# Optimization experiments

Hardware: AMD Instinct MI355X
Metric: run time of the kernel (lower is better)

## Reference

```python
import jax, jax.numpy as jnp
import numpy as np

B, H, W = 16, 352, 352
EPS = 1e-7

# Directable[TL_table[i]] for i = 0..7: (dx, dy), dx=+1 shifts right, dy=+1 shifts down
# TL_table = [lower_right, down, lower_left, right, left, upper_right, up, upper_left]
SHIFTS = [(1, 1), (0, 1), (-1, 1), (1, 0), (-1, 0), (1, -1), (0, -1), (-1, -1)]


def _shift(x, dx, dy):
    # x: [B,H,W]; zero-padded translation, equivalent to the bmm against the
    # near-identity translation matrices in the original code.
    if dx == 1:
        x = jnp.pad(x, ((0, 0), (0, 0), (1, 0)))[:, :, :-1]
    elif dx == -1:
        x = jnp.pad(x, ((0, 0), (0, 0), (0, 1)))[:, :, 1:]
    if dy == 1:
        x = jnp.pad(x, ((0, 0), (1, 0), (0, 0)))[:, :-1, :]
    elif dy == -1:
        x = jnp.pad(x, ((0, 0), (0, 1), (0, 0)))[:, 1:, :]
    return x


def _bce_sum(p, t):
    p = jnp.clip(p, EPS, 1.0 - EPS)
    return -jnp.sum(t * jnp.log(p) + (1.0 - t) * jnp.log1p(-p))


def setup_inputs() -> dict:
    key = jax.random.key(0)
    k1, k2, k3 = jax.random.split(key, 3)
    c_map = jax.random.normal(k1, (B, 8, H, W), dtype=jnp.float32)
    target = jax.random.uniform(k2, (B, 1, H, W), dtype=jnp.float32)
    con_target = jax.random.randint(k3, (B, 8, H, W), 0, 2, dtype=jnp.int32)
    return {"c_map": c_map, "target": target, "con_target": con_target}


def reference(c_map, target, con_target):
    p = jax.nn.sigmoid(c_map)                      # [B,8,H,W]
    con = con_target.astype(p.dtype)
    sum_conn = jnp.sum(con, axis=1)                # [B,H,W]
    edge = ((sum_conn < 8) & (sum_conn > 0)).astype(p.dtype)

    # Bilateral voting: shifted[:, i] = shift(p[:, 7-i], direction_i)
    shifted = jnp.stack(
        [_shift(p[:, 7 - i], *SHIFTS[i]) for i in range(8)], axis=1
    )                                              # [B,8,H,W]
    vote = p * shifted                             # [B,8,H,W]

    glo_map = jnp.max(vote, axis=1)                # [B,H,W]
    pred_mask_min = jnp.min(vote, axis=1)          # [B,H,W]
    decouple = glo_map * (1.0 - edge) + (1.0 - pred_mask_min) * edge

    de_loss = _bce_sum(decouple[:, None], target)
    conmap_l = _bce_sum(p, con)
    bimap_l = _bce_sum(vote, con)
    return 0.8 * conmap_l + de_loss + 0.2 * bimap_l
```

## Files before the change

### kernel.cpp

```cpp
#include <hip/hip_runtime.h>


#define EPSF 1e-7f

constexpr int B = 16, H = 352, W = 352;
constexpr int HW = H * W;
constexpr int N = B * HW;
constexpr int W4 = W / 4;
constexpr int HW4 = HW / 4;
constexpr int NQ = N / 4;
constexpr int NBLK = NQ / 256;

typedef float f4 __attribute__((ext_vector_type(4)));
typedef int   i4 __attribute__((ext_vector_type(4)));

__device__ __forceinline__ float rcpf(float x) { return __builtin_amdgcn_rcpf(x); }

__device__ __forceinline__ f4 sigmoid4(f4 x) {
    f4 r;
    r.x = rcpf(1.0f + __expf(-x.x));
    r.y = rcpf(1.0f + __expf(-x.y));
    r.z = rcpf(1.0f + __expf(-x.z));
    r.w = rcpf(1.0f + __expf(-x.w));
    return r;
}
__device__ __forceinline__ f4 max4(f4 a, f4 b) {
    f4 r; r.x=fmaxf(a.x,b.x); r.y=fmaxf(a.y,b.y); r.z=fmaxf(a.z,b.z); r.w=fmaxf(a.w,b.w); return r;
}
__device__ __forceinline__ f4 min4(f4 a, f4 b) {
    f4 r; r.x=fminf(a.x,b.x); r.y=fminf(a.y,b.y); r.z=fminf(a.z,b.z); r.w=fminf(a.w,b.w); return r;
}
__device__ __forceinline__ f4 sel4(i4 q, f4 a, f4 b) {
    f4 r; r.x=q.x?a.x:b.x; r.y=q.y?a.y:b.y; r.z=q.z?a.z:b.z; r.w=q.w?a.w:b.w; return r;
}
__device__ __forceinline__ f4 loadu4(const float* p) {
    f4 v; __builtin_memcpy(&v, p, sizeof(f4)); return v;
}

__device__ __forceinline__ float finish_pixel(float glo, float pmin, int sc,
                                              float t, float cp, float ba, float bb) {
    const float edge = (sc < 8 && sc > 0) ? 1.0f : 0.0f;
    float dec = glo * (1.0f - edge) + (1.0f - pmin) * edge;
    dec = fminf(fmaxf(dec, EPSF), 1.0f - EPSF);
    const float de = -(t * __logf(dec) + (1.0f - t) * __logf(1.0f - dec));
    return de - 0.8f * __logf(cp) - 0.2f * (__logf(ba) + __logf(bb));
}

__global__ __launch_bounds__(256, 4) void bicon_loss_kernel(
    const float* __restrict__ c_map,
    const float* __restrict__ target,
    const int*   __restrict__ con,
    float* __restrict__ ws)
{
    const int tid = blockIdx.x * blockDim.x + threadIdx.x;
    const int b  = tid / HW4;
    const int rq = tid - b * HW4;
    const int y  = rq / W4;
    const int xq = rq - y * W4;
    const int x0 = xq * 4;

    const float* __restrict__ cm = c_map + (size_t)b * 8 * HW + y * W + x0;
    const int*   __restrict__ cn = con   + (size_t)b * 8 * HW + y * W + x0;

    const f4 c0 = *(const f4*)(cm + 0 * HW);
    const f4 c1 = *(const f4*)(cm + 1 * HW);
    const f4 c2 = *(const f4*)(cm + 2 * HW);
    const f4 c3 = *(const f4*)(cm + 3 * HW);
    const f4 c4 = *(const f4*)(cm + 4 * HW);
    const f4 c5 = *(const f4*)(cm + 5 * HW);
    const f4 c6 = *(const f4*)(cm + 6 * HW);
    const f4 c7 = *(const f4*)(cm + 7 * HW);
    const f4 n0 = loadu4(cm + 7 * HW - 1 * W - 1);
    const f4 n1 = *(const f4*)(cm + 6 * HW - 1 * W);
    const f4 n2 = loadu4(cm + 5 * HW - 1 * W + 1);
    const f4 n3 = loadu4(cm + 4 * HW - 1);
    const f4 n4 = loadu4(cm + 3 * HW + 1);
    const f4 n5 = loadu4(cm + 2 * HW + 1 * W - 1);
    const f4 n6 = *(const f4*)(cm + 1 * HW + 1 * W);
    const f4 n7 = loadu4(cm + 0 * HW + 1 * W + 1);
    const i4 q0 = *(const i4*)(cn + 0 * HW);
    const i4 q1 = *(const i4*)(cn + 1 * HW);
    const i4 q2 = *(const i4*)(cn + 2 * HW);
    const i4 q3 = *(const i4*)(cn + 3 * HW);
    const i4 q4 = *(const i4*)(cn + 4 * HW);
    const i4 q5 = *(const i4*)(cn + 5 * HW);
    const i4 q6 = *(const i4*)(cn + 6 * HW);
    const i4 q7 = *(const i4*)(cn + 7 * HW);
    const f4 t4 = *(const f4*)(target + (size_t)b * HW + y * W + x0);

    const f4 p0 = sigmoid4(c0);
    const f4 p1 = sigmoid4(c1);
    const f4 p2 = sigmoid4(c2);
    const f4 p3 = sigmoid4(c3);
    const f4 p4 = sigmoid4(c4);
    const f4 p5 = sigmoid4(c5);
    const f4 p6 = sigmoid4(c6);
    const f4 p7 = sigmoid4(c7);

    const float lm = (xq == 0)      ? 0.0f : 1.0f;
    const float rm = (xq == W4 - 1) ? 0.0f : 1.0f;
    const float tm = (y == 0)       ? 0.0f : 1.0f;
    const float bm = (y == H - 1)   ? 0.0f : 1.0f;

    f4 conprod = {1.f,1.f,1.f,1.f};
    f4 biA     = {1.f,1.f,1.f,1.f};
    f4 biB     = {1.f,1.f,1.f,1.f};
    f4 glo     = {-1e30f,-1e30f,-1e30f,-1e30f};
    f4 pmin    = { 1e30f, 1e30f, 1e30f, 1e30f};

#define DIR(P, Q, NR, DX, RMASK, BI) {                                        \
        f4 s = sigmoid4(NR);                                                  \
        s *= (RMASK);                                                         \
        if ((DX) == 1)  s.x *= lm;                                            \
        if ((DX) == -1) s.w *= rm;                                            \
        const f4 v = (P) * s;                                                 \
        glo  = max4(glo,  v);                                                 \
        pmin = min4(pmin, v);                                                 \
        conprod *= sel4((Q), (P), 1.0f - (P));                                \
        BI *= sel4((Q), max4(v, (f4){EPSF,EPSF,EPSF,EPSF}), 1.0f - v);        \
    }
    DIR(p0, q0, n0,  1, tm, biA)
    DIR(p1, q1, n1,  0, tm, biA)
    DIR(p2, q2, n2, -1, tm, biA)
    DIR(p3, q3, n3,  1, 1.0f, biA)
    DIR(p4, q4, n4, -1, 1.0f, biB)
    DIR(p5, q5, n5,  1, bm, biB)
    DIR(p6, q6, n6,  0, bm, biB)
    DIR(p7, q7, n7, -1, bm, biB)
#undef DIR

    const i4 sc = q0 + q1 + q2 + q3 + q4 + q5 + q6 + q7;

    float part = finish_pixel(glo.x, pmin.x, sc.x, t4.x, conprod.x, biA.x, biB.x)
               + finish_pixel(glo.y, pmin.y, sc.y, t4.y, conprod.y, biA.y, biB.y)
               + finish_pixel(glo.z, pmin.z, sc.z, t4.z, conprod.z, biA.z, biB.z)
               + finish_pixel(glo.w, pmin.w, sc.w, t4.w, conprod.w, biA.w, biB.w);

    #pragma unroll
    for (int off = 32; off > 0; off >>= 1)
        part += __shfl_down(part, off, 64);

    __shared__ float wsum[4];
    const int lane = threadIdx.x & 63;
    const int wid  = threadIdx.x >> 6;
    if (lane == 0) wsum[wid] = part;
    __syncthreads();
    if (threadIdx.x == 0) {
        ws[blockIdx.x] = wsum[0] + wsum[1] + wsum[2] + wsum[3];
    }
}

__global__ __launch_bounds__(256) void reduce_partials_kernel(
    const float* __restrict__ ws, float* __restrict__ out)
{
    float s = 0.0f;
    for (int i = threadIdx.x; i < NBLK; i += 256) s += ws[i];
    #pragma unroll
    for (int off = 32; off > 0; off >>= 1)
        s += __shfl_down(s, off, 64);
    __shared__ float wsum[4];
    const int lane = threadIdx.x & 63;
    const int wid  = threadIdx.x >> 6;
    if (lane == 0) wsum[wid] = s;
    __syncthreads();
    if (threadIdx.x == 0) out[0] = wsum[0] + wsum[1] + wsum[2] + wsum[3];
}

extern "C" void kernel_launch(void* const* d_in, const int* in_sizes, int n_in,
                              void* d_out, int out_size, void* d_ws, size_t ws_size,
                              hipStream_t stream) {
    const float* c_map  = (const float*)d_in[0];
    const float* target = (const float*)d_in[1];
    const int*   con    = (const int*)d_in[2];
    float* out = (float*)d_out;
    float* ws  = (float*)d_ws;

    bicon_loss_kernel<<<NBLK, 256, 0, stream>>>(c_map, target, con, ws);
    reduce_partials_kernel<<<1, 256, 0, stream>>>(ws, out);
}
```

Before: 149.4 us.

## Process four-row strips per thread with rolling sigmoid window and lane shuffles

Each thread now walks four consecutive rows instead of one pixel quad. Sigmoid values for the previous, current and next rows are carried in registers and reused across rows, so each input element gets its sigmoid once instead of twice. Horizontal neighbours come from cross-lane shuffles, with scalar fix-up loads only at wavefront edges, replacing the unaligned global loads. The trade-off is a grid four times smaller (484 blocks), which means less latency hiding and more register pressure per thread.

Measured after the change: 167.4 us. +12.1%, slower.

```diff
diff --git a/kernel.cpp b/kernel.cpp
--- a/kernel.cpp
+++ b/kernel.cpp
@@ -3,18 +3,21 @@
 
 #define EPSF 1e-7f
 
-constexpr int B = 16, H = 352, W = 352;
+constexpr int B_ = 16, H = 352, W = 352;
 constexpr int HW = H * W;
-constexpr int N = B * HW;
 constexpr int W4 = W / 4;
-constexpr int HW4 = HW / 4;
-constexpr int NQ = N / 4;
-constexpr int NBLK = NQ / 256;
+constexpr int RPT = 4;
+constexpr int STRIPS = H / RPT;
+constexpr int SPB = STRIPS * W4;
+constexpr int NT = B_ * SPB;
+constexpr int BLK = 256;
+constexpr int NBLK = NT / BLK;
 
 typedef float f4 __attribute__((ext_vector_type(4)));
 typedef int   i4 __attribute__((ext_vector_type(4)));
 
 __device__ __forceinline__ float rcpf(float x) { return __builtin_amdgcn_rcpf(x); }
+__device__ __forceinline__ float sigf(float x) { return rcpf(1.0f + __expf(-x)); }
 
 __device__ __forceinline__ f4 sigmoid4(f4 x) {
     f4 r;
@@ -33,8 +36,18 @@
 __device__ __forceinline__ f4 sel4(i4 q, f4 a, f4 b) {
     f4 r; r.x=q.x?a.x:b.x; r.y=q.y?a.y:b.y; r.z=q.z?a.z:b.z; r.w=q.w?a.w:b.w; return r;
 }
-__device__ __forceinline__ f4 loadu4(const float* p) {
-    f4 v; __builtin_memcpy(&v, p, sizeof(f4)); return v;
+__device__ __forceinline__ f4 ld4(const float* p) { return *(const f4*)p; }
+__device__ __forceinline__ i4 ldi4(const int* p)  { return *(const i4*)p; }
+
+__device__ __forceinline__ f4 shiftR4(f4 p, float fixL, bool isLane0) {
+    float left = __shfl_up(p.w, 1, 64);
+    if (isLane0) left = fixL;
+    f4 r; r.x = left; r.y = p.x; r.z = p.y; r.w = p.z; return r;
+}
+__device__ __forceinline__ f4 shiftL4(f4 p, float fixR, bool isLane63) {
+    float right = __shfl_down(p.x, 1, 64);
+    if (isLane63) right = fixR;
+    f4 r; r.x = p.y; r.y = p.z; r.z = p.w; r.w = right; return r;
 }
 
 __device__ __forceinline__ float finish_pixel(float glo, float pmin, int sc,
@@ -46,70 +59,110 @@
     return de - 0.8f * __logf(cp) - 0.2f * (__logf(ba) + __logf(bb));
 }
 
-__global__ __launch_bounds__(256, 4) void bicon_loss_kernel(
+__global__ __launch_bounds__(BLK) void bicon_r13_main(
     const float* __restrict__ c_map,
     const float* __restrict__ target,
     const int*   __restrict__ con,
     float* __restrict__ ws)
 {
-    const int tid = blockIdx.x * blockDim.x + threadIdx.x;
-    const int b  = tid / HW4;
-    const int rq = tid - b * HW4;
-    const int y  = rq / W4;
-    const int xq = rq - y * W4;
-    const int x0 = xq * 4;
-
-    const float* __restrict__ cm = c_map + (size_t)b * 8 * HW + y * W + x0;
-    const int*   __restrict__ cn = con   + (size_t)b * 8 * HW + y * W + x0;
-
-    const f4 c0 = *(const f4*)(cm + 0 * HW);
-    const f4 c1 = *(const f4*)(cm + 1 * HW);
-    const f4 c2 = *(const f4*)(cm + 2 * HW);
-    const f4 c3 = *(const f4*)(cm + 3 * HW);
-    const f4 c4 = *(const f4*)(cm + 4 * HW);
-    const f4 c5 = *(const f4*)(cm + 5 * HW);
-    const f4 c6 = *(const f4*)(cm + 6 * HW);
-    const f4 c7 = *(const f4*)(cm + 7 * HW);
-    const f4 n0 = loadu4(cm + 7 * HW - 1 * W - 1);
-    const f4 n1 = *(const f4*)(cm + 6 * HW - 1 * W);
-    const f4 n2 = loadu4(cm + 5 * HW - 1 * W + 1);
-    const f4 n3 = loadu4(cm + 4 * HW - 1);
-    const f4 n4 = loadu4(cm + 3 * HW + 1);
-    const f4 n5 = loadu4(cm + 2 * HW + 1 * W - 1);
-    const f4 n6 = *(const f4*)(cm + 1 * HW + 1 * W);
-    const f4 n7 = loadu4(cm + 0 * HW + 1 * W + 1);
-    const i4 q0 = *(const i4*)(cn + 0 * HW);
-    const i4 q1 = *(const i4*)(cn + 1 * HW);
-    const i4 q2 = *(const i4*)(cn + 2 * HW);
-    const i4 q3 = *(const i4*)(cn + 3 * HW);
-    const i4 q4 = *(const i4*)(cn + 4 * HW);
-    const i4 q5 = *(const i4*)(cn + 5 * HW);
-    const i4 q6 = *(const i4*)(cn + 6 * HW);
-    const i4 q7 = *(const i4*)(cn + 7 * HW);
-    const f4 t4 = *(const f4*)(target + (size_t)b * HW + y * W + x0);
-
-    const f4 p0 = sigmoid4(c0);
-    const f4 p1 = sigmoid4(c1);
-    const f4 p2 = sigmoid4(c2);
-    const f4 p3 = sigmoid4(c3);
-    const f4 p4 = sigmoid4(c4);
-    const f4 p5 = sigmoid4(c5);
-    const f4 p6 = sigmoid4(c6);
-    const f4 p7 = sigmoid4(c7);
+    const int tid   = blockIdx.x * BLK + threadIdx.x;
+    const int b     = tid / SPB;
+    const int rem   = tid - b * SPB;
+    const int strip = rem / W4;
+    const int xq    = rem - strip * W4;
+    const int x0    = xq * 4;
+    const int y0    = strip * RPT;
+    const int lane  = threadIdx.x & 63;
+
+    const float* __restrict__ cmb = c_map + (size_t)b * 8 * HW;
+    const int*   __restrict__ cnb = con   + (size_t)b * 8 * HW;
+    const float* __restrict__ tb  = target + (size_t)b * HW;
 
     const float lm = (xq == 0)      ? 0.0f : 1.0f;
     const float rm = (xq == W4 - 1) ? 0.0f : 1.0f;
-    const float tm = (y == 0)       ? 0.0f : 1.0f;
-    const float bm = (y == H - 1)   ? 0.0f : 1.0f;
-
-    f4 conprod = {1.f,1.f,1.f,1.f};
-    f4 biA     = {1.f,1.f,1.f,1.f};
-    f4 biB     = {1.f,1.f,1.f,1.f};
-    f4 glo     = {-1e30f,-1e30f,-1e30f,-1e30f};
-    f4 pmin    = { 1e30f, 1e30f, 1e30f, 1e30f};
-
-#define DIR(P, Q, NR, DX, RMASK, BI) {                                        \
-        f4 s = sigmoid4(NR);                                                  \
+
+    const int ypr = (y0 > 0) ? y0 - 1 : 0;
+    f4 pp5 = sigmoid4(ld4(cmb + 5 * HW + ypr * W + x0));
+    f4 pp6 = sigmoid4(ld4(cmb + 6 * HW + ypr * W + x0));
+    f4 pp7 = sigmoid4(ld4(cmb + 7 * HW + ypr * W + x0));
+    f4 p0 = sigmoid4(ld4(cmb + 0 * HW + y0 * W + x0));
+    f4 p1 = sigmoid4(ld4(cmb + 1 * HW + y0 * W + x0));
+    f4 p2 = sigmoid4(ld4(cmb + 2 * HW + y0 * W + x0));
+    f4 p3 = sigmoid4(ld4(cmb + 3 * HW + y0 * W + x0));
+    f4 p4 = sigmoid4(ld4(cmb + 4 * HW + y0 * W + x0));
+    f4 p5 = sigmoid4(ld4(cmb + 5 * HW + y0 * W + x0));
+    f4 p6 = sigmoid4(ld4(cmb + 6 * HW + y0 * W + x0));
+    f4 p7 = sigmoid4(ld4(cmb + 7 * HW + y0 * W + x0));
+
+    float part = 0.0f;
+
+    #pragma unroll
+    for (int r = 0; r < RPT; ++r) {
+        const bool fullPrefetch = (r != RPT - 1);
+        const int y  = y0 + r;
+        const int yn = (y + 1 < H) ? y + 1 : y;
+        const int ypc = (y > 0) ? y - 1 : 0;
+        const float* cyn = cmb + yn * W + x0;
+
+        const f4 cn0 = ld4(cyn + 0 * HW);
+        const f4 cn1 = ld4(cyn + 1 * HW);
+        const f4 cn2 = ld4(cyn + 2 * HW);
+        f4 cn3{}, cn4{}, cn5{}, cn6{}, cn7{};
+        if (fullPrefetch) {
+            cn3 = ld4(cyn + 3 * HW);
+            cn4 = ld4(cyn + 4 * HW);
+            cn5 = ld4(cyn + 5 * HW);
+            cn6 = ld4(cyn + 6 * HW);
+            cn7 = ld4(cyn + 7 * HW);
+        }
+        const int* qy = cnb + y * W + x0;
+        const i4 q0 = ldi4(qy + 0 * HW);
+        const i4 q1 = ldi4(qy + 1 * HW);
+        const i4 q2 = ldi4(qy + 2 * HW);
+        const i4 q3 = ldi4(qy + 3 * HW);
+        const i4 q4 = ldi4(qy + 4 * HW);
+        const i4 q5 = ldi4(qy + 5 * HW);
+        const i4 q6 = ldi4(qy + 6 * HW);
+        const i4 q7 = ldi4(qy + 7 * HW);
+        const f4 t4 = ld4(tb + y * W + x0);
+
+        float fA = 0.f, fB = 0.f, fC = 0.f, fD = 0.f, fE = 0.f, fF = 0.f;
+        if (lane == 0) {
+            const int xl = (xq == 0) ? x0 : x0 - 1;
+            fA = sigf(cmb[7 * HW + ypc * W + xl]);
+            fB = sigf(cmb[4 * HW + y   * W + xl]);
+            fC = sigf(cmb[2 * HW + yn  * W + xl]);
+        } else if (lane == 63) {
+            const int xr = (xq == W4 - 1) ? x0 + 3 : x0 + 4;
+            fD = sigf(cmb[5 * HW + ypc * W + xr]);
+            fE = sigf(cmb[3 * HW + y   * W + xr]);
+            fF = sigf(cmb[0 * HW + yn  * W + xr]);
+        }
+
+        const f4 pn0 = sigmoid4(cn0);
+        const f4 pn1 = sigmoid4(cn1);
+        const f4 pn2 = sigmoid4(cn2);
+
+        const float tm = (y == 0)     ? 0.0f : 1.0f;
+        const float bm = (y == H - 1) ? 0.0f : 1.0f;
+
+        const f4 s0 = shiftR4(pp7, fA, lane == 0);
+        const f4 s1 = pp6;
+        const f4 s2 = shiftL4(pp5, fD, lane == 63);
+        const f4 s3 = shiftR4(p4,  fB, lane == 0);
+        const f4 s4 = shiftL4(p3,  fE, lane == 63);
+        const f4 s5 = shiftR4(pn2, fC, lane == 0);
+        const f4 s6 = pn1;
+        const f4 s7 = shiftL4(pn0, fF, lane == 63);
+
+        f4 conprod = {1.f,1.f,1.f,1.f};
+        f4 biA     = {1.f,1.f,1.f,1.f};
+        f4 biB     = {1.f,1.f,1.f,1.f};
+        f4 glo     = {-1e30f,-1e30f,-1e30f,-1e30f};
+        f4 pmin    = { 1e30f, 1e30f, 1e30f, 1e30f};
+
+#define DIR(P, Q, S, DX, RMASK, BI) {                                         \
+        f4 s = (S);                                                           \
         s *= (RMASK);                                                         \
         if ((DX) == 1)  s.x *= lm;                                            \
         if ((DX) == -1) s.w *= rm;                                            \
@@ -119,30 +172,40 @@
         conprod *= sel4((Q), (P), 1.0f - (P));                                \
         BI *= sel4((Q), max4(v, (f4){EPSF,EPSF,EPSF,EPSF}), 1.0f - v);        \
     }
-    DIR(p0, q0, n0,  1, tm, biA)
-    DIR(p1, q1, n1,  0, tm, biA)
-    DIR(p2, q2, n2, -1, tm, biA)
-    DIR(p3, q3, n3,  1, 1.0f, biA)
-    DIR(p4, q4, n4, -1, 1.0f, biB)
-    DIR(p5, q5, n5,  1, bm, biB)
-    DIR(p6, q6, n6,  0, bm, biB)
-    DIR(p7, q7, n7, -1, bm, biB)
+        DIR(p0, q0, s0,  1, tm, biA)
+        DIR(p1, q1, s1,  0, tm, biA)
+        DIR(p2, q2, s2, -1, tm, biA)
+        DIR(p3, q3, s3,  1, 1.0f, biA)
+        DIR(p4, q4, s4, -1, 1.0f, biB)
+        DIR(p5, q5, s5,  1, bm, biB)
+        DIR(p6, q6, s6,  0, bm, biB)
+        DIR(p7, q7, s7, -1, bm, biB)
 #undef DIR
 
-    const i4 sc = q0 + q1 + q2 + q3 + q4 + q5 + q6 + q7;
-
-    float part = finish_pixel(glo.x, pmin.x, sc.x, t4.x, conprod.x, biA.x, biB.x)
-               + finish_pixel(glo.y, pmin.y, sc.y, t4.y, conprod.y, biA.y, biB.y)
-               + finish_pixel(glo.z, pmin.z, sc.z, t4.z, conprod.z, biA.z, biB.z)
-               + finish_pixel(glo.w, pmin.w, sc.w, t4.w, conprod.w, biA.w, biB.w);
+        const i4 sc = q0 + q1 + q2 + q3 + q4 + q5 + q6 + q7;
+
+        part += finish_pixel(glo.x, pmin.x, sc.x, t4.x, conprod.x, biA.x, biB.x)
+              + finish_pixel(glo.y, pmin.y, sc.y, t4.y, conprod.y, biA.y, biB.y)
+              + finish_pixel(glo.z, pmin.z, sc.z, t4.z, conprod.z, biA.z, biB.z)
+              + finish_pixel(glo.w, pmin.w, sc.w, t4.w, conprod.w, biA.w, biB.w);
+
+        pp5 = p5; pp6 = p6; pp7 = p7;
+        p0 = pn0; p1 = pn1; p2 = pn2;
+        if (fullPrefetch) {
+            p3 = sigmoid4(cn3);
+            p4 = sigmoid4(cn4);
+            p5 = sigmoid4(cn5);
+            p6 = sigmoid4(cn6);
+            p7 = sigmoid4(cn7);
+        }
+    }
 
     #pragma unroll
     for (int off = 32; off > 0; off >>= 1)
         part += __shfl_down(part, off, 64);
 
     __shared__ float wsum[4];
-    const int lane = threadIdx.x & 63;
-    const int wid  = threadIdx.x >> 6;
+    const int wid = threadIdx.x >> 6;
     if (lane == 0) wsum[wid] = part;
     __syncthreads();
     if (threadIdx.x == 0) {
@@ -150,7 +213,7 @@
     }
 }
 
-__global__ __launch_bounds__(256) void reduce_partials_kernel(
+__global__ __launch_bounds__(256) void bicon_r13_reduce(
     const float* __restrict__ ws, float* __restrict__ out)
 {
     float s = 0.0f;
@@ -175,6 +238,6 @@
     float* out = (float*)d_out;
     float* ws  = (float*)d_ws;
 
-    bicon_loss_kernel<<<NBLK, 256, 0, stream>>>(c_map, target, con, ws);
-    reduce_partials_kernel<<<1, 256, 0, stream>>>(ws, out);
-}
+    bicon_r13_main<<<NBLK, BLK, 0, stream>>>(c_map, target, con, ws);
+    bicon_r13_reduce<<<1, 256, 0, stream>>>(ws, out);
+}
```

## Stage sigmoid planes in LDS per row strip to reuse neighbour loads

Applied to the files above, without the earlier changes.

Each 704-thread block now handles an 8-row strip of one image. It loads the needed c_map channel rows, including a one-row halo, applies the sigmoid once and stores the results in shared memory in two phases. Neighbour shifts are then read from LDS instead of being reloaded unaligned from global memory with a second sigmoid, which removes redundant global traffic and duplicate exp work. In exchange it adds barriers, about 60KB of LDS per block that limits occupancy, and halo reloads at strip edges.

Result: slower. 156.1 us (+4.5%).

```diff
diff --git a/kernel.cpp b/kernel.cpp
--- a/kernel.cpp
+++ b/kernel.cpp
@@ -3,13 +3,18 @@
 
 #define EPSF 1e-7f
 
-constexpr int B = 16, H = 352, W = 352;
+constexpr int B_ = 16, H = 352, W = 352;
 constexpr int HW = H * W;
-constexpr int N = B * HW;
-constexpr int W4 = W / 4;
-constexpr int HW4 = HW / 4;
-constexpr int NQ = N / 4;
-constexpr int NBLK = NQ / 256;
+constexpr int W4 = 88;
+constexpr int RPB = 8;
+constexpr int BLK = 704;
+constexpr int STRIPS = H / RPB;
+constexpr int NBLK = B_ * STRIPS;
+constexpr int PLN = 352;
+constexpr int NPLANE_A = 43;
+constexpr int NPLANE_B = 27;
+constexpr int SLOTS_A = NPLANE_A * W4;
+constexpr int SLOTS_B = NPLANE_B * W4;
 
 typedef float f4 __attribute__((ext_vector_type(4)));
 typedef int   i4 __attribute__((ext_vector_type(4)));
@@ -33,9 +38,8 @@
 __device__ __forceinline__ f4 sel4(i4 q, f4 a, f4 b) {
     f4 r; r.x=q.x?a.x:b.x; r.y=q.y?a.y:b.y; r.z=q.z?a.z:b.z; r.w=q.w?a.w:b.w; return r;
 }
-__device__ __forceinline__ f4 loadu4(const float* p) {
-    f4 v; __builtin_memcpy(&v, p, sizeof(f4)); return v;
-}
+__device__ __forceinline__ f4 ld4(const float* p) { return *(const f4*)p; }
+__device__ __forceinline__ i4 ldi4(const int* p)  { return *(const i4*)p; }
 
 __device__ __forceinline__ float finish_pixel(float glo, float pmin, int sc,
                                               float t, float cp, float ba, float bb) {
@@ -46,61 +50,79 @@
     return de - 0.8f * __logf(cp) - 0.2f * (__logf(ba) + __logf(bb));
 }
 
-__global__ __launch_bounds__(256, 4) void bicon_loss_kernel(
+#define DIR(P, Q, S, DX, RMASK, BI) {                                         \
+        f4 s_ = (S);                                                          \
+        s_ *= (RMASK);                                                        \
+        if ((DX) == 1)  s_.x *= lm;                                           \
+        if ((DX) == -1) s_.w *= rm;                                           \
+        const f4 v = (P) * s_;                                                \
+        glo  = max4(glo,  v);                                                 \
+        pmin = min4(pmin, v);                                                 \
+        conprod *= sel4((Q), (P), 1.0f - (P));                                \
+        BI *= sel4((Q), max4(v, (f4){EPSF,EPSF,EPSF,EPSF}), 1.0f - v);        \
+    }
+
+__global__ __launch_bounds__(BLK) void bicon_r15_main(
     const float* __restrict__ c_map,
     const float* __restrict__ target,
     const int*   __restrict__ con,
     float* __restrict__ ws)
 {
-    const int tid = blockIdx.x * blockDim.x + threadIdx.x;
-    const int b  = tid / HW4;
-    const int rq = tid - b * HW4;
-    const int y  = rq / W4;
-    const int xq = rq - y * W4;
-    const int x0 = xq * 4;
-
-    const float* __restrict__ cm = c_map + (size_t)b * 8 * HW + y * W + x0;
-    const int*   __restrict__ cn = con   + (size_t)b * 8 * HW + y * W + x0;
-
-    const f4 c0 = *(const f4*)(cm + 0 * HW);
-    const f4 c1 = *(const f4*)(cm + 1 * HW);
-    const f4 c2 = *(const f4*)(cm + 2 * HW);
-    const f4 c3 = *(const f4*)(cm + 3 * HW);
-    const f4 c4 = *(const f4*)(cm + 4 * HW);
-    const f4 c5 = *(const f4*)(cm + 5 * HW);
-    const f4 c6 = *(const f4*)(cm + 6 * HW);
-    const f4 c7 = *(const f4*)(cm + 7 * HW);
-    const f4 n0 = loadu4(cm + 7 * HW - 1 * W - 1);
-    const f4 n1 = *(const f4*)(cm + 6 * HW - 1 * W);
-    const f4 n2 = loadu4(cm + 5 * HW - 1 * W + 1);
-    const f4 n3 = loadu4(cm + 4 * HW - 1);
-    const f4 n4 = loadu4(cm + 3 * HW + 1);
-    const f4 n5 = loadu4(cm + 2 * HW + 1 * W - 1);
-    const f4 n6 = *(const f4*)(cm + 1 * HW + 1 * W);
-    const f4 n7 = loadu4(cm + 0 * HW + 1 * W + 1);
-    const i4 q0 = *(const i4*)(cn + 0 * HW);
-    const i4 q1 = *(const i4*)(cn + 1 * HW);
-    const i4 q2 = *(const i4*)(cn + 2 * HW);
-    const i4 q3 = *(const i4*)(cn + 3 * HW);
-    const i4 q4 = *(const i4*)(cn + 4 * HW);
-    const i4 q5 = *(const i4*)(cn + 5 * HW);
-    const i4 q6 = *(const i4*)(cn + 6 * HW);
-    const i4 q7 = *(const i4*)(cn + 7 * HW);
-    const f4 t4 = *(const f4*)(target + (size_t)b * HW + y * W + x0);
-
-    const f4 p0 = sigmoid4(c0);
-    const f4 p1 = sigmoid4(c1);
-    const f4 p2 = sigmoid4(c2);
-    const f4 p3 = sigmoid4(c3);
-    const f4 p4 = sigmoid4(c4);
-    const f4 p5 = sigmoid4(c5);
-    const f4 p6 = sigmoid4(c6);
-    const f4 p7 = sigmoid4(c7);
-
-    const float lm = (xq == 0)      ? 0.0f : 1.0f;
-    const float rm = (xq == W4 - 1) ? 0.0f : 1.0f;
+    __shared__ float lds[NPLANE_A * PLN];
+
+    const int bi    = blockIdx.x;
+    const int b     = bi / STRIPS;
+    const int strip = bi - b * STRIPS;
+    const int ty0   = strip * RPB;
+    const int tid   = threadIdx.x;
+    const int row   = tid / W4;
+    const int qc    = tid - row * W4;
+    const int x0    = qc * 4;
+    const int y     = ty0 + row;
+
+    const float* __restrict__ cmb = c_map + (size_t)b * 8 * HW;
+    const int*   __restrict__ cnb = con   + (size_t)b * 8 * HW;
+    const float* __restrict__ tb  = target + (size_t)b * HW;
+
+    #pragma unroll
+    for (int k = 0; k < 6; ++k) {
+        const int s = tid + k * BLK;
+        if (s < SLOTS_A) {
+            const int plane = s / W4;
+            const int qs    = s - plane * W4;
+            int ch, r;
+            if (plane < 27) { ch = 5 + plane / 9; r = plane % 9 - 1; }
+            else            { const int p2 = plane - 27; ch = 3 + (p2 >> 3); r = p2 & 7; }
+            int g = ty0 + r; g = (g < 0) ? 0 : ((g > H - 1) ? H - 1 : g);
+            const f4 v = sigmoid4(ld4(cmb + ch * HW + g * W + qs * 4));
+            *(f4*)&lds[plane * PLN + qs * 4] = v;
+        }
+    }
+    const i4 q3 = ldi4(cnb + 3 * HW + y * W + x0);
+    const i4 q4 = ldi4(cnb + 4 * HW + y * W + x0);
+    const f4 t4 = ld4(tb + y * W + x0);
+    __syncthreads();
+
+    const float lm = (qc == 0)      ? 0.0f : 1.0f;
+    const float rm = (qc == W4 - 1) ? 0.0f : 1.0f;
     const float tm = (y == 0)       ? 0.0f : 1.0f;
     const float bm = (y == H - 1)   ? 0.0f : 1.0f;
+    const int xl = (x0 > 0) ? x0 - 1 : 0;
+    const int xr = (x0 + 4 < W) ? x0 + 4 : W - 1;
+
+    f4 C;
+    C = *(const f4*)&lds[(18 + row) * PLN + x0];
+    f4 S0 = {lds[(18 + row) * PLN + xl], C.x, C.y, C.z};
+    f4 S1 = *(const f4*)&lds[(9 + row) * PLN + x0];
+    C = *(const f4*)&lds[(0 + row) * PLN + x0];
+    f4 S2 = {C.y, C.z, C.w, lds[(0 + row) * PLN + xr]};
+    const f4 p5 = *(const f4*)&lds[(0 + row + 1) * PLN + x0];
+    const f4 p6 = *(const f4*)&lds[(9 + row + 1) * PLN + x0];
+    const f4 p7 = *(const f4*)&lds[(18 + row + 1) * PLN + x0];
+    const f4 p3 = *(const f4*)&lds[(27 + row) * PLN + x0];
+    const f4 p4 = *(const f4*)&lds[(35 + row) * PLN + x0];
+    const f4 S3 = {lds[(35 + row) * PLN + xl], p4.x, p4.y, p4.z};
+    const f4 S4 = {p3.y, p3.z, p3.w, lds[(27 + row) * PLN + xr]};
 
     f4 conprod = {1.f,1.f,1.f,1.f};
     f4 biA     = {1.f,1.f,1.f,1.f};
@@ -108,28 +130,49 @@
     f4 glo     = {-1e30f,-1e30f,-1e30f,-1e30f};
     f4 pmin    = { 1e30f, 1e30f, 1e30f, 1e30f};
 
-#define DIR(P, Q, NR, DX, RMASK, BI) {                                        \
-        f4 s = sigmoid4(NR);                                                  \
-        s *= (RMASK);                                                         \
-        if ((DX) == 1)  s.x *= lm;                                            \
-        if ((DX) == -1) s.w *= rm;                                            \
-        const f4 v = (P) * s;                                                 \
-        glo  = max4(glo,  v);                                                 \
-        pmin = min4(pmin, v);                                                 \
-        conprod *= sel4((Q), (P), 1.0f - (P));                                \
-        BI *= sel4((Q), max4(v, (f4){EPSF,EPSF,EPSF,EPSF}), 1.0f - v);        \
-    }
-    DIR(p0, q0, n0,  1, tm, biA)
-    DIR(p1, q1, n1,  0, tm, biA)
-    DIR(p2, q2, n2, -1, tm, biA)
-    DIR(p3, q3, n3,  1, 1.0f, biA)
-    DIR(p4, q4, n4, -1, 1.0f, biB)
-    DIR(p5, q5, n5,  1, bm, biB)
-    DIR(p6, q6, n6,  0, bm, biB)
-    DIR(p7, q7, n7, -1, bm, biB)
-#undef DIR
-
-    const i4 sc = q0 + q1 + q2 + q3 + q4 + q5 + q6 + q7;
+    DIR(p3, q3, S3,  1, 1.0f, biA)
+    DIR(p4, q4, S4, -1, 1.0f, biB)
+    i4 sc = q3 + q4;
+
+    __syncthreads();
+
+    #pragma unroll
+    for (int k = 0; k < 4; ++k) {
+        const int s = tid + k * BLK;
+        if (s < SLOTS_B) {
+            const int plane = s / W4;
+            const int qs    = s - plane * W4;
+            const int ch = plane / 9;
+            const int r  = plane - ch * 9;
+            int g = ty0 + r; g = (g > H - 1) ? H - 1 : g;
+            const f4 v = sigmoid4(ld4(cmb + ch * HW + g * W + qs * 4));
+            *(f4*)&lds[plane * PLN + qs * 4] = v;
+        }
+    }
+    const i4 q0 = ldi4(cnb + 0 * HW + y * W + x0);
+    const i4 q1 = ldi4(cnb + 1 * HW + y * W + x0);
+    const i4 q2 = ldi4(cnb + 2 * HW + y * W + x0);
+    const i4 q5 = ldi4(cnb + 5 * HW + y * W + x0);
+    const i4 q6 = ldi4(cnb + 6 * HW + y * W + x0);
+    const i4 q7 = ldi4(cnb + 7 * HW + y * W + x0);
+    __syncthreads();
+
+    const f4 p0 = *(const f4*)&lds[(0 + row) * PLN + x0];
+    const f4 p1 = *(const f4*)&lds[(9 + row) * PLN + x0];
+    const f4 p2 = *(const f4*)&lds[(18 + row) * PLN + x0];
+    C = *(const f4*)&lds[(18 + row + 1) * PLN + x0];
+    const f4 S5 = {lds[(18 + row + 1) * PLN + xl], C.x, C.y, C.z};
+    const f4 S6 = *(const f4*)&lds[(9 + row + 1) * PLN + x0];
+    C = *(const f4*)&lds[(0 + row + 1) * PLN + x0];
+    const f4 S7 = {C.y, C.z, C.w, lds[(0 + row + 1) * PLN + xr]};
+
+    DIR(p0, q0, S0,  1, tm, biA)
+    DIR(p1, q1, S1,  0, tm, biA)
+    DIR(p2, q2, S2, -1, tm, biA)
+    DIR(p5, q5, S5,  1, bm, biB)
+    DIR(p6, q6, S6,  0, bm, biB)
+    DIR(p7, q7, S7, -1, bm, biB)
+    sc += q0 + q1 + q2 + q5 + q6 + q7;
 
     float part = finish_pixel(glo.x, pmin.x, sc.x, t4.x, conprod.x, biA.x, biB.x)
                + finish_pixel(glo.y, pmin.y, sc.y, t4.y, conprod.y, biA.y, biB.y)
@@ -140,17 +183,20 @@
     for (int off = 32; off > 0; off >>= 1)
         part += __shfl_down(part, off, 64);
 
-    __shared__ float wsum[4];
-    const int lane = threadIdx.x & 63;
-    const int wid  = threadIdx.x >> 6;
+    __shared__ float wsum[11];
+    const int lane = tid & 63;
+    const int wid  = tid >> 6;
     if (lane == 0) wsum[wid] = part;
     __syncthreads();
-    if (threadIdx.x == 0) {
-        ws[blockIdx.x] = wsum[0] + wsum[1] + wsum[2] + wsum[3];
-    }
-}
-
-__global__ __launch_bounds__(256) void reduce_partials_kernel(
+    if (tid == 0) {
+        float s = 0.0f;
+        #pragma unroll
+        for (int w = 0; w < 11; ++w) s += wsum[w];
+        ws[bi] = s;
+    }
+}
+
+__global__ __launch_bounds__(256) void bicon_r15_reduce(
     const float* __restrict__ ws, float* __restrict__ out)
 {
     float s = 0.0f;
@@ -175,6 +221,6 @@
     float* out = (float*)d_out;
     float* ws  = (float*)d_ws;
 
-    bicon_loss_kernel<<<NBLK, 256, 0, stream>>>(c_map, target, con, ws);
-    reduce_partials_kernel<<<1, 256, 0, stream>>>(ws, out);
-}
+    bicon_r15_main<<<NBLK, BLK, 0, stream>>>(c_map, target, con, ws);
+    bicon_r15_reduce<<<1, 256, 0, stream>>>(ws, out);
+}
```
